# Optimization experiments

Measured on AMD Instinct MI355X. Metric: run time of the kernel, lower is better.

The kernel has to match this reference:

```python
import jax, jax.numpy as jnp
from jax import lax
import numpy as np

STRIDE = 1
PADDING = 1
DILATION = 1


def setup_inputs() -> dict:
    key = jax.random.key(0)
    k1, k2, k3, k4 = jax.random.split(key, 4)
    B, Cin, Cout, H, W, K, G = 32, 256, 256, 56, 56, 3, 8
    x = jax.random.normal(k1, (B, Cin, H, W), dtype=jnp.float32)
    conv = jax.random.normal(k2, (Cout, Cin, K, K), dtype=jnp.float32)
    S = jax.random.normal(k3, (Cin, G), dtype=jnp.float32)
    T = jax.random.normal(k4, (Cout, G), dtype=jnp.float32)
    return {"x": x, "conv": conv, "S": S, "T": T}


def reference(x, conv, S, T):
    # Faithful to FLGC.forward (training path).
    Cin = S.shape[0]
    Cout = T.shape[0]
    s_hat = jax.nn.softmax(S, axis=1)            # [Cin, G]
    t_hat = jax.nn.softmax(T, axis=1)            # [Cout, G]
    s = jnp.argmax(s_hat, axis=1)                # group id per input channel
    t = jnp.argmax(t_hat, axis=1)                # group id per output filter
    # Input channel c is scaled by s_hat[c, s[c]] inside its group.
    x_sc = x * s_hat[jnp.arange(Cin), s][None, :, None, None]
    # Filter o uses weight conv[o,c] * t_hat[o, t[o]] only where s[c] == t[o];
    # masking weights to zero elsewhere makes one dense conv equal the per-group convs.
    gate = (s[None, :] == t[:, None]).astype(conv.dtype)          # [Cout, Cin]
    w = conv * t_hat[jnp.arange(Cout), t][:, None, None, None] * gate[:, :, None, None]
    out_full = lax.conv_general_dilated(
        x_sc, w,
        window_strides=(STRIDE, STRIDE),
        padding=[(PADDING, PADDING), (PADDING, PADDING)],
        rhs_dilation=(DILATION, DILATION),
    )  # [B, Cout, H', W'], channel o = group-conv output of filter o
    # Original concatenates group outputs (channels ordered by perm = stable sort of t),
    # then indexes that with perm again: final[:, j] = out_full[:, perm[perm[j]]].
    perm = jnp.argsort(t * Cout + jnp.arange(Cout))  # stable group-major order
    return out_full[:, perm[perm]]
```

## Files before the change

### kernel.cpp

```cpp
#include <hip/hip_runtime.h>

#define M_SI    0
#define M_SO    256
#define M_CLIST 512
#define M_FLIST 768
#define M_DEST  1024
#define M_CBASE 1280
#define M_FBASE 1288
#define M_CCNT  1296
#define M_FCNT  1304
#define M_WOFFE 1312
#define WPACK_BYTE_OFF 16384
#define XR_BYTE_OFF   (4u << 20)
#define SLOT_ELEMS    3444736ull
#define SLOT_BYTES    (SLOT_ELEMS * 2ull)

typedef short bf16x8 __attribute__((ext_vector_type(8)));
typedef float f32x4  __attribute__((ext_vector_type(4)));

__device__ __forceinline__ unsigned short f2bf(float f) {
    unsigned u = __float_as_uint(f);
    u += 0x7fffu + ((u >> 16) & 1u);
    return (unsigned short)(u >> 16);
}

__device__ __forceinline__ void gl_lds16(const void* g, void* l) {
    __builtin_amdgcn_global_load_lds((const __attribute__((address_space(1))) unsigned int*)g,
                                     (__attribute__((address_space(3))) unsigned int*)l, 16, 0, 0);
}

__global__ __launch_bounds__(256) void flgc_setup(const float* __restrict__ S,
                                                  const float* __restrict__ T,
                                                  int* __restrict__ meta) {
    __shared__ float si[256], so[256];
    __shared__ int gin[256], gout[256];
    __shared__ int cnt_in[8], cnt_out[8], cb[8], fb[8];
    __shared__ int perm[256], destl[256];
    const int c = threadIdx.x;

    {
        float m = S[c * 8]; int am = 0;
        for (int k = 1; k < 8; ++k) { float v = S[c * 8 + k]; if (v > m) { m = v; am = k; } }
        float s = 0.f;
        for (int k = 0; k < 8; ++k) s += expf(S[c * 8 + k] - m);
        si[c] = 1.0f / s; gin[c] = am;
    }
    {
        float m = T[c * 8]; int am = 0;
        for (int k = 1; k < 8; ++k) { float v = T[c * 8 + k]; if (v > m) { m = v; am = k; } }
        float s = 0.f;
        for (int k = 0; k < 8; ++k) s += expf(T[c * 8 + k] - m);
        so[c] = 1.0f / s; gout[c] = am;
    }
    __syncthreads();
    const int g = gin[c], go = gout[c];
    int r1 = 0, r2 = 0;
    for (int i = 0; i < c; ++i) { r1 += (gin[i] == g); r2 += (gout[i] == go); }
    if (c < 8) {
        int n1 = 0, n2 = 0;
        for (int i = 0; i < 256; ++i) { n1 += (gin[i] == c); n2 += (gout[i] == c); }
        cnt_in[c] = n1; cnt_out[c] = n2;
    }
    __syncthreads();
    if (c == 0) {
        int a = 0, b = 0;
        for (int k = 0; k < 8; ++k) { cb[k] = a; a += cnt_in[k]; fb[k] = b; b += cnt_out[k]; }
    }
    __syncthreads();
    meta[M_CLIST + cb[g] + r1] = c;
    perm[fb[go] + r2] = c;
    __syncthreads();
    const int ppc = perm[perm[c]];
    destl[ppc] = c;
    __syncthreads();
    ((float*)meta)[M_SI + c] = si[c];
    ((float*)meta)[M_SO + c] = so[c];
    meta[M_FLIST + c] = perm[c];
    meta[M_DEST + c]  = destl[c];
    if (c < 8) {
        meta[M_CBASE + c] = cb[c];
        meta[M_FBASE + c] = fb[c];
        meta[M_CCNT + c]  = cnt_in[c];
        meta[M_FCNT + c]  = cnt_out[c];
    }
    if (c == 0) {
        int a = 0;
        for (int k = 0; k < 8; ++k) {
            meta[M_WOFFE + k] = a;
            const int nq  = (cnt_in[k] + 31) >> 5;
            const int mfa = (cnt_out[k] + 15) >> 4;
            a += nq * mfa * 9 * 512;
        }
        meta[M_WOFFE + 8] = a;
    }
}

__global__ void flgc_pack(const float* __restrict__ conv, const int* __restrict__ meta,
                          unsigned short* __restrict__ wpack) {
    const float* si = (const float*)meta + M_SI;
    const float* so = (const float*)meta + M_SO;
    const int total = meta[M_WOFFE + 8];
    for (int idx = blockIdx.x * blockDim.x + threadIdx.x; idx < total;
         idx += gridDim.x * blockDim.x) {
        int gg = 0;
        while (gg < 7 && idx >= meta[M_WOFFE + gg + 1]) ++gg;
        const int local = idx - meta[M_WOFFE + gg];
        const int fcnt = meta[M_FCNT + gg], ccnt = meta[M_CCNT + gg];
        const int mfall = (fcnt + 15) >> 4;
        const int fragidx = local >> 9, e = local & 511;
        const int lane = e >> 3, j = e & 7;
        const int tap = fragidx % 9, t2 = fragidx / 9;
        const int mf = t2 % mfall, q = t2 / mfall;
        const int fl = mf * 16 + (lane & 15);
        const int cl = q * 32 + (lane >> 4) * 8 + j;
        float v = 0.f;
        if (fl < fcnt && cl < ccnt) {
            const int F  = meta[M_FLIST + meta[M_FBASE + gg] + fl];
            const int CH = meta[M_CLIST + meta[M_CBASE + gg] + cl];
            v = conv[(F * 256 + CH) * 9 + tap] * si[CH] * so[F];
        }
        wpack[idx] = f2bf(v);
    }
}

__global__ __launch_bounds__(256) void flgc_reorder(const float* __restrict__ x,
                                                    const int* __restrict__ meta,
                                                    unsigned short* __restrict__ xr) {
    const int bx = blockIdx.x;
    const int b = blockIdx.y;
    const int slot = blockIdx.z;
    const int g = slot >> 1, q = slot & 1;
    const int ccnt = meta[M_CCNT + g];
    int nq = (ccnt + 31) >> 5; if (nq > 2) nq = 2;
    if (q >= nq) return;
    const int cbas = meta[M_CBASE + g];
    const int tid = threadIdx.x;
    const int chu = tid & 7;
    const int a   = (tid >> 3) & 15;
    const int rr  = 2 * bx + (tid >> 7);
    const int xrow = rr - 1;

    int chn[4];
#pragma unroll
    for (int i = 0; i < 4; ++i) {
        const int cgl = q * 32 + chu * 4 + i;
        chn[i] = (cgl < ccnt) ? meta[M_CLIST + cbas + cgl] : -1;
    }
    float4 v[4];
#pragma unroll
    for (int i = 0; i < 4; ++i) v[i] = make_float4(0.f, 0.f, 0.f, 0.f);
    if ((unsigned)xrow < 56u && a < 14) {
        const float* xb = x + (size_t)b * 256 * 3136 + xrow * 56 + a * 4;
#pragma unroll
        for (int i = 0; i < 4; ++i)
            if (chn[i] >= 0) v[i] = *(const float4*)(xb + (size_t)chn[i] * 3136);
    }
    unsigned short* dst = xr + (size_t)(slot * 32 + b) * 107648ull + (size_t)rr * 1856;
    const int c16 = chu >> 1, lo = (chu & 1) * 4;
    if (a < 14) {
#define PACKK(comp, kk)                                                                   \
        {                                                                                 \
            const int col = 4 * a + 1 + (kk);                                             \
            const int s16 = c16 ^ ((col >> 1) & 3);                                       \
            ushort4 pk = make_ushort4(f2bf(v[0].comp), f2bf(v[1].comp),                   \
                                      f2bf(v[2].comp), f2bf(v[3].comp));                  \
            *(ushort4*)&dst[col * 32 + s16 * 8 + lo] = pk;                                \
        }
        PACKK(x, 0) PACKK(y, 1) PACKK(z, 2) PACKK(w, 3)
#undef PACKK
    } else {
        const int col = (a == 14) ? 0 : 57;
        const int s16 = c16 ^ ((col >> 1) & 3);
        *(ushort4*)&dst[col * 32 + s16 * 8 + lo] = make_ushort4(0, 0, 0, 0);
    }
}

template <int MFE>
__device__ __forceinline__ void conv_pass(
    const unsigned short* __restrict__ wpack, const unsigned short* __restrict__ xr,
    float* __restrict__ out, unsigned short* xbufA, unsigned short* xbufB,
    const int (&ocv)[3][4], int b, int g, int z, int nq, int mf0, int mfall, int woffe,
    int lane, int wv) {
    const int nn = lane & 15, kg = lane >> 4;
    int addrc[4][3];
#pragma unroll
    for (int cg = 0; cg < 4; ++cg)
#pragma unroll
        for (int dc = 0; dc < 3; ++dc) {
            int ccol = cg * 16 + nn + dc; if (ccol > 57) ccol = 57;
            addrc[cg][dc] = (ccol << 6) + ((kg ^ ((ccol >> 1) & 3)) << 4);
        }
    const int ns = (z < 2) ? 4 : 3;
    const int P = ns * nq;
    const int base = wv * 348;
    {
        const char* src = (const char*)(xr + (size_t)((g * 2) * 32 + b) * 107648ull
                                        + (size_t)(4 * z) * 1856);
        char* dstb = (char*)xbufA;
#pragma unroll
        for (int j = 0; j < 5; ++j)
            gl_lds16(src + (size_t)(base + j * 64 + lane) * 16, dstb + (base + j * 64) * 16);
        if (lane < 28)
            gl_lds16(src + (size_t)(base + 320 + lane) * 16, dstb + (base + 320) * 16);
    }
    f32x4 acc[MFE][4];
    for (int p = 0; p < P; ++p) {
        const int q = (nq == 2) ? (p & 1) : 0;
        const int s = z + 4 * ((nq == 2) ? (p >> 1) : p);
        bf16x8 A[MFE][9];
        {
            const unsigned short* ap =
                wpack + woffe + ((size_t)(q * mfall + mf0) * 9) * 512 + lane * 8;
#pragma unroll
            for (int mf = 0; mf < MFE; ++mf)
#pragma unroll
                for (int tap = 0; tap < 9; ++tap)
                    A[mf][tap] = *(const bf16x8*)(ap + (size_t)(mf * 9 + tap) * 512);
        }
        __builtin_amdgcn_sched_barrier(0);
        if (p + 1 < P) {
            const int pn = p + 1;
            const int qp = (nq == 2) ? (pn & 1) : 0;
            const int sp = z + 4 * ((nq == 2) ? (pn >> 1) : pn);
            const char* src = (const char*)(xr + (size_t)((g * 2 + qp) * 32 + b) * 107648ull
                                            + (size_t)(4 * sp) * 1856);
            char* dstb = (char*)((pn & 1) ? xbufB : xbufA);
#pragma unroll
            for (int j = 0; j < 5; ++j)
                gl_lds16(src + (size_t)(base + j * 64 + lane) * 16, dstb + (base + j * 64) * 16);
            if (lane < 28)
                gl_lds16(src + (size_t)(base + 320 + lane) * 16, dstb + (base + 320) * 16);
            asm volatile("s_waitcnt vmcnt(6)" ::: "memory");
        } else {
            asm volatile("s_waitcnt vmcnt(0)" ::: "memory");
        }
        __builtin_amdgcn_s_barrier();
        __builtin_amdgcn_sched_barrier(0);
        const unsigned short* xb = (p & 1) ? xbufB : xbufA;
        if (q == 0) {
#pragma unroll
            for (int mf = 0; mf < MFE; ++mf)
#pragma unroll
                for (int cg = 0; cg < 4; ++cg) acc[mf][cg] = (f32x4){0.f, 0.f, 0.f, 0.f};
        }
#pragma unroll
        for (int tap = 0; tap < 9; ++tap) {
            const int dr = tap / 3, dc = tap - dr * 3;
            const int rowb = ((wv + dr) * 58) << 6;
#pragma unroll
            for (int cg = 0; cg < 4; ++cg) {
                const bf16x8 Bv = *(const bf16x8*)((const char*)xb + rowb + addrc[cg][dc]);
#pragma unroll
                for (int mf = 0; mf < MFE; ++mf)
                    acc[mf][cg] = __builtin_amdgcn_mfma_f32_16x16x32_bf16(
                        A[mf][tap], Bv, acc[mf][cg], 0, 0, 0);
            }
        }
        if (q == nq - 1) {
            const int h = 4 * s + wv;
#pragma unroll
            for (int mf = 0; mf < MFE; ++mf)
#pragma unroll
                for (int reg = 0; reg < 4; ++reg) {
                    const int oc = ocv[mf][reg];
                    if (oc >= 0) {
                        float* op = out + ((size_t)(b * 256 + oc) * 56 + h) * 56;
#pragma unroll
                        for (int cg = 0; cg < 4; ++cg) {
                            const int col = cg * 16 + nn;
                            if (col < 56) op[col] = acc[mf][cg][reg];
                        }
                    }
                }
        }
        __builtin_amdgcn_sched_barrier(0);
        __builtin_amdgcn_s_barrier();
    }
}

__global__ __launch_bounds__(256, 2) void flgc_conv_r(const int* __restrict__ meta,
                                                      const unsigned short* __restrict__ wpack,
                                                      const unsigned short* __restrict__ xr,
                                                      float* __restrict__ out) {
    __shared__ __align__(16) unsigned short xbufA[11136];
    __shared__ __align__(16) unsigned short xbufB[11136];
    const int b = blockIdx.x, g = blockIdx.y, z = blockIdx.z;
    const int tid = threadIdx.x, lane = tid & 63, wv = tid >> 6;
    const int ccnt = meta[M_CCNT + g], fcnt = meta[M_FCNT + g];
    const int fbas = meta[M_FBASE + g], woffe = meta[M_WOFFE + g];
    int nq = (ccnt + 31) >> 5; if (nq > 2) nq = 2;
    const int mfall = (fcnt + 15) >> 4;
    if (mfall == 0) return;
    const int nn = lane & 15;

    for (int mf0 = 0; mf0 < mfall; mf0 += 3) {
        const int mfe = min(3, mfall - mf0);
        int ocv[3][4];
#pragma unroll
        for (int mf = 0; mf < 3; ++mf)
#pragma unroll
            for (int reg = 0; reg < 4; ++reg) {
                const int fl = (mf0 + mf) * 16 + (lane >> 4) * 4 + reg;
                ocv[mf][reg] = (mf < mfe && fl < fcnt)
                    ? meta[M_DEST + meta[M_FLIST + fbas + fl]] : -1;
            }
        if (nq == 0) {
            const int ns = (z < 2) ? 4 : 3;
            for (int si = 0; si < ns; ++si) {
                const int h = 4 * (z + 4 * si) + wv;
#pragma unroll
                for (int mf = 0; mf < 3; ++mf)
#pragma unroll
                    for (int reg = 0; reg < 4; ++reg)
                        if (ocv[mf][reg] >= 0) {
                            float* op = out + ((size_t)(b * 256 + ocv[mf][reg]) * 56 + h) * 56;
#pragma unroll
                            for (int cg = 0; cg < 4; ++cg) {
                                const int col = cg * 16 + nn;
                                if (col < 56) op[col] = 0.f;
                            }
                        }
            }
            continue;
        }
        if (mfe == 3)      conv_pass<3>(wpack, xr, out, xbufA, xbufB, ocv, b, g, z, nq, mf0, mfall, woffe, lane, wv);
        else if (mfe == 2) conv_pass<2>(wpack, xr, out, xbufA, xbufB, ocv, b, g, z, nq, mf0, mfall, woffe, lane, wv);
        else               conv_pass<1>(wpack, xr, out, xbufA, xbufB, ocv, b, g, z, nq, mf0, mfall, woffe, lane, wv);
    }
}

__global__ __launch_bounds__(256, 2) void flgc_conv_mfma(const float* __restrict__ x,
                                                         const int* __restrict__ meta,
                                                         const unsigned short* __restrict__ wpack,
                                                         float* __restrict__ out) {
    __shared__ __align__(16) unsigned short xlds[10 * 4 * 64 * 8];
    __shared__ __align__(16) unsigned short wlds[4 * 9 * 512];
    const int g = blockIdx.z, b = blockIdx.y, h0 = blockIdx.x * 8;
    const int tid = threadIdx.x, lane = tid & 63, wv = tid >> 6;
    const int ccnt = meta[M_CCNT + g], fcnt = meta[M_FCNT + g];
    const int cbas = meta[M_CBASE + g], fbas = meta[M_FBASE + g];
    const int woffe = meta[M_WOFFE + g];
    const int nq = (ccnt + 31) >> 5, mfall = (fcnt + 15) >> 4;
    if (mfall == 0) return;
    const int n = lane & 15, kgl = lane >> 4;
    const int prow = 2 * wv + (n >> 3);
    const int pcol = n & 7;

    for (int mf0 = 0; mf0 < mfall; mf0 += 4) {
        const int mfe = min(4, mfall - mf0);
        f32x4 acc[4][7];
#pragma unroll
        for (int mf = 0; mf < 4; ++mf)
#pragma unroll
            for (int cg = 0; cg < 7; ++cg) acc[mf][cg] = (f32x4){0.f, 0.f, 0.f, 0.f};

        for (int q = 0; q < nq; ++q) {
            __syncthreads();
            for (int widx = wv; widx < mfe * 9; widx += 4) {
                const int mf = widx / 9, tap = widx - mf * 9;
                const unsigned short* src =
                    wpack + woffe + (((q * mfall) + mf0 + mf) * 9 + tap) * 512 + lane * 8;
                *(bf16x8*)&wlds[(mf * 9 + tap) * 512 + lane * 8] = *(const bf16x8*)src;
            }
            for (int i = tid; i < 80 * 64; i += 256) {
                const int colx = i & 63, t = i >> 6;
                const int rr = t >> 3, cq = t & 7;
                const int c0 = q * 32 + cq * 4;
                const int row = h0 + rr - 1, ic = colx - 1;
                float v0 = 0.f, v1 = 0.f, v2 = 0.f, v3 = 0.f;
                if ((unsigned)row < 56u && (unsigned)ic < 56u) {
                    const float* xp = x + (size_t)(b * 256) * 3136 + row * 56 + ic;
                    if (c0 + 0 < ccnt) v0 = xp[(size_t)meta[M_CLIST + cbas + c0 + 0] * 3136];
                    if (c0 + 1 < ccnt) v1 = xp[(size_t)meta[M_CLIST + cbas + c0 + 1] * 3136];
                    if (c0 + 2 < ccnt) v2 = xp[(size_t)meta[M_CLIST + cbas + c0 + 2] * 3136];
                    if (c0 + 3 < ccnt) v3 = xp[(size_t)meta[M_CLIST + cbas + c0 + 3] * 3136];
                }
                ushort4 pk = make_ushort4(f2bf(v0), f2bf(v1), f2bf(v2), f2bf(v3));
                *(ushort4*)&xlds[(((rr * 4 + (cq >> 1)) * 64 + colx) << 3) + ((cq & 1) << 2)] = pk;
            }
            __syncthreads();
#pragma unroll
            for (int tap = 0; tap < 9; ++tap) {
                const int dr = tap / 3, dcp = tap - dr * 3;
                bf16x8 A[4];
#pragma unroll
                for (int mf = 0; mf < 4; ++mf)
                    if (mf < mfe)
                        A[mf] = *(bf16x8*)&wlds[(mf * 9 + tap) * 512 + lane * 8];
                const int row_r = prow + dr;
                const int xbase = ((row_r * 4 + kgl) * 64) << 3;
#pragma unroll
                for (int cg = 0; cg < 7; ++cg) {
                    const int cc = cg * 8 + pcol + dcp;
                    const bf16x8 B = *(bf16x8*)&xlds[xbase + (cc << 3)];
#pragma unroll
                    for (int mf = 0; mf < 4; ++mf)
                        if (mf < mfe)
                            acc[mf][cg] = __builtin_amdgcn_mfma_f32_16x16x32_bf16(
                                A[mf], B, acc[mf][cg], 0, 0, 0);
                }
            }
        }
#pragma unroll
        for (int mf = 0; mf < 4; ++mf) {
            if (mf < mfe) {
#pragma unroll
                for (int reg = 0; reg < 4; ++reg) {
                    const int fl = (mf0 + mf) * 16 + (lane >> 4) * 4 + reg;
                    if (fl < fcnt) {
                        const int F  = meta[M_FLIST + fbas + fl];
                        const int oc = meta[M_DEST + F];
                        float* op = out + ((size_t)(b * 256 + oc) * 56 + (h0 + prow)) * 56 + pcol;
#pragma unroll
                        for (int cg = 0; cg < 7; ++cg)
                            op[cg * 8] = acc[mf][cg][reg];
                    }
                }
            }
        }
    }
}

extern "C" void kernel_launch(void* const* d_in, const int* in_sizes, int n_in,
                              void* d_out, int out_size, void* d_ws, size_t ws_size,
                              hipStream_t stream) {
    const float* x    = (const float*)d_in[0];
    const float* conv = (const float*)d_in[1];
    const float* S    = (const float*)d_in[2];
    const float* T    = (const float*)d_in[3];
    float* out = (float*)d_out;
    int* meta = (int*)d_ws;
    unsigned short* wpack = (unsigned short*)((char*)d_ws + WPACK_BYTE_OFF);
    unsigned short* xr    = (unsigned short*)((char*)d_ws + XR_BYTE_OFF);

    flgc_setup<<<1, 256, 0, stream>>>(S, T, meta);
    flgc_pack<<<256, 256, 0, stream>>>(conv, meta, wpack);

    const size_t need = (size_t)XR_BYTE_OFF + 16ull * SLOT_BYTES + 65536;
    if (ws_size >= need) {
        flgc_reorder<<<dim3(29, 32, 16), 256, 0, stream>>>(x, meta, xr);
        flgc_conv_r<<<dim3(32, 8, 4), 256, 0, stream>>>(meta, wpack, xr, out);
    } else {
        flgc_conv_mfma<<<dim3(7, 32, 8), 256, 0, stream>>>(x, meta, wpack, out);
    }
}
```

Measured before the change: 107.4 us.

## Stage reorder kernel input through LDS with direct global-to-LDS loads

The channel-reorder/bf16-pack kernel now has each block load four rows of 32 gathered channels into shared memory via gl_lds16 direct-to-LDS loads, then converts and writes the swizzled bf16 layout from LDS. Each block covers four output rows instead of two, so the grid shrinks from 29 to 15 blocks in x. The intent is more coalesced, latency-hidden global reads for the gather. The cost is 33 KB of LDS per block and an extra barrier. Padding rows and channels are handled by clamping loads and zeroing values afterward.

```diff
diff --git a/kernel.cpp b/kernel.cpp
--- a/kernel.cpp
+++ b/kernel.cpp
@@ -126,6 +126,7 @@
 __global__ __launch_bounds__(256) void flgc_reorder(const float* __restrict__ x,
                                                     const int* __restrict__ meta,
                                                     unsigned short* __restrict__ xr) {
+    __shared__ __align__(16) float lds[8448];
     const int bx = blockIdx.x;
     const int b = blockIdx.y;
     const int slot = blockIdx.z;
@@ -134,44 +135,56 @@
     int nq = (ccnt + 31) >> 5; if (nq > 2) nq = 2;
     if (q >= nq) return;
     const int cbas = meta[M_CBASE + g];
-    const int tid = threadIdx.x;
-    const int chu = tid & 7;
-    const int a   = (tid >> 3) & 15;
-    const int rr  = 2 * bx + (tid >> 7);
-    const int xrow = rr - 1;
-
-    int chn[4];
-#pragma unroll
-    for (int i = 0; i < 4; ++i) {
-        const int cgl = q * 32 + chu * 4 + i;
-        chn[i] = (cgl < ccnt) ? meta[M_CLIST + cbas + cgl] : -1;
-    }
-    float4 v[4];
-#pragma unroll
-    for (int i = 0; i < 4; ++i) v[i] = make_float4(0.f, 0.f, 0.f, 0.f);
-    if ((unsigned)xrow < 56u && a < 14) {
-        const float* xb = x + (size_t)b * 256 * 3136 + xrow * 56 + a * 4;
-#pragma unroll
-        for (int i = 0; i < 4; ++i)
-            if (chn[i] >= 0) v[i] = *(const float4*)(xb + (size_t)chn[i] * 3136);
-    }
-    unsigned short* dst = xr + (size_t)(slot * 32 + b) * 107648ull + (size_t)rr * 1856;
-    const int c16 = chu >> 1, lo = (chu & 1) * 4;
-    if (a < 14) {
-#define PACKK(comp, kk)                                                                   \
-        {                                                                                 \
-            const int col = 4 * a + 1 + (kk);                                             \
-            const int s16 = c16 ^ ((col >> 1) & 3);                                       \
-            ushort4 pk = make_ushort4(f2bf(v[0].comp), f2bf(v[1].comp),                   \
-                                      f2bf(v[2].comp), f2bf(v[3].comp));                  \
-            *(ushort4*)&dst[col * 32 + s16 * 8 + lo] = pk;                                \
-        }
-        PACKK(x, 0) PACKK(y, 1) PACKK(z, 2) PACKK(w, 3)
-#undef PACKK
-    } else {
-        const int col = (a == 14) ? 0 : 57;
-        const int s16 = c16 ^ ((col >> 1) & 3);
-        *(ushort4*)&dst[col * 32 + s16 * 8 + lo] = make_ushort4(0, 0, 0, 0);
+    const int tid = threadIdx.x, lane = tid & 63, wv = tid >> 6;
+
+    {
+        const int xrow0 = 4 * bx + wv - 1;
+        const int xrow = (xrow0 < 0) ? 0 : ((xrow0 > 55) ? 55 : xrow0);
+        const int i = lane >> 4;
+        int col4 = (lane & 15) * 4; if (col4 > 52) col4 = 52;
+        const float* xb = x + (size_t)b * 802816 + (size_t)xrow * 56 + col4;
+        for (int j = 0; j < 8; ++j) {
+            const int cgl = q * 32 + 4 * j + i;
+            const int ch = meta[M_CLIST + cbas + ((cgl < ccnt) ? cgl : 0)];
+            gl_lds16(xb + (size_t)ch * 3136, (char*)lds + (wv * 8 + j) * 1056);
+        }
+    }
+    __syncthreads();
+
+    unsigned short* dstb = xr + (size_t)(slot * 32 + b) * 107648ull;
+    if (tid < 32) {
+        const int rr = tid >> 3, rem = tid & 7;
+        const int r = 4 * bx + rr;
+        if (r < 58) {
+            const int col = (rem >> 2) ? 57 : 0;
+            const int sl = rem & 3;
+            *(ushort4*)&dstb[(size_t)r * 1856 + col * 32 + sl * 4] = make_ushort4(0, 0, 0, 0);
+        }
+    }
+    for (int k = tid; k < 448; k += 256) {
+        const int rr = k / 112, rem = k - rr * 112;
+        const int chq = rem / 14, aq = rem - chq * 14;
+        const int r = 4 * bx + rr;
+        if (r >= 58) continue;
+        const int xrow0 = r - 1;
+        const bool rowok = (unsigned)xrow0 < 56u;
+        f32x4 vv[4];
+#pragma unroll
+        for (int i = 0; i < 4; ++i) {
+            vv[i] = *(const f32x4*)&lds[(rr * 8 + chq) * 264 + i * 64 + 4 * aq];
+            const int cgl = q * 32 + 4 * chq + i;
+            if (!rowok || cgl >= ccnt) vv[i] = (f32x4){0.f, 0.f, 0.f, 0.f};
+        }
+        const int c16 = chq >> 1, lo = (chq & 1) * 4;
+        unsigned short* dr = dstb + (size_t)r * 1856;
+#pragma unroll
+        for (int kk = 0; kk < 4; ++kk) {
+            const int col = 4 * aq + 1 + kk;
+            const int s16 = c16 ^ ((col >> 1) & 3);
+            ushort4 pk = make_ushort4(f2bf(vv[0][kk]), f2bf(vv[1][kk]),
+                                      f2bf(vv[2][kk]), f2bf(vv[3][kk]));
+            *(ushort4*)&dr[col * 32 + s16 * 8 + lo] = pk;
+        }
     }
 }
 
@@ -438,7 +451,7 @@
 
     const size_t need = (size_t)XR_BYTE_OFF + 16ull * SLOT_BYTES + 65536;
     if (ws_size >= need) {
-        flgc_reorder<<<dim3(29, 32, 16), 256, 0, stream>>>(x, meta, xr);
+        flgc_reorder<<<dim3(15, 32, 16), 256, 0, stream>>>(x, meta, xr);
         flgc_conv_r<<<dim3(32, 8, 4), 256, 0, stream>>>(meta, wpack, xr, out);
     } else {
         flgc_conv_mfma<<<dim3(7, 32, 8), 256, 0, stream>>>(x, meta, wpack, out);
```

Result: slower. 111.6 us (+3.9%).
